# Performance work log

Measured on AMD Instinct MI355X. Metric: run time of the kernel, lower is better.

The kernel has to match this reference:

```python
import jax, jax.numpy as jnp
import numpy as np

WINDOW = 8  # outlier_fraction = 0.125 -> 1 fp column kept per 8-wide window

# XnorBinaryLinear's STEBinary: sign in fwd, identity (straight-through) in bwd
@jax.custom_vjp
def ste_sign(x):
    return jnp.sign(x)

def _ste_fwd(x):
    return jnp.sign(x), None

def _ste_bwd(_, g):
    return (g,)

ste_sign.defvjp(_ste_fwd, _ste_bwd)


def quant_weight(w):
    # XnorBinaryLinear.quant_weight: per-row mean-center, sign, rescale by
    # detached per-row mean absolute value
    mu = jnp.mean(w, axis=-1, keepdims=True)
    wc = w - mu
    scale = jax.lax.stop_gradient(jnp.mean(jnp.abs(wc), axis=-1, keepdims=True))
    return ste_sign(wc) * scale


def binarize_except_outliers(w):
    # Binarize weight, then restore the max-|w| element of each flat 8-wide
    # window to full precision (calibration = argmax of |w| per window,
    # identical to outlier_calibration with L1 metric on first forward).
    wq = quant_weight(w)
    wv = w.reshape(-1, WINDOW)             # [n_windows, 8]
    idx = jnp.argmax(jnp.abs(wv), axis=1)  # [n_windows] outlier column per window
    mask = jnp.arange(WINDOW)[None, :] == idx[:, None]  # one-hot bool mask
    out = jnp.where(mask, wv, wq.reshape(-1, WINDOW))
    return out.reshape(w.shape)


def setup_inputs() -> dict:
    key = jax.random.key(0)
    k1, k2, k3 = jax.random.split(key, 3)
    x = jax.random.normal(k1, (4, 2048, 4096), dtype=jnp.float32)
    weight = jax.random.normal(k2, (4096, 4096), dtype=jnp.float32) * 0.02
    bias = jax.random.normal(k3, (4096,), dtype=jnp.float32) * 0.02
    return {"x": x, "weight": weight, "bias": bias}


def reference(x, weight, bias):
    w = binarize_except_outliers(weight)     # [OC, IC]
    return jnp.einsum('bsi,oi->bso', x, w) + bias
```

## Files before the change

### kernel.cpp

```cpp
#include <hip/hip_runtime.h>
#include <stdint.h>

#define M_DIM 8192
#define N_DIM 4096
#define K_DIM 4096

#define BM 256
#define BN 128
#define BK 32
#define NT (K_DIM / BK)

typedef float v4f __attribute__((ext_vector_type(4)));
typedef __bf16 v8bf __attribute__((ext_vector_type(8)));

typedef __attribute__((address_space(3))) uint32_t lds_u32_t;
typedef const __attribute__((address_space(1))) uint32_t glb_u32_t;

__device__ inline uint16_t f2bf(float f) {
    union { float f; uint32_t u; } v; v.f = f;
    uint32_t r = v.u + 0x7fffu + ((v.u >> 16) & 1u);
    return (uint16_t)(r >> 16);
}

__global__ __launch_bounds__(256) void cvt_x(const float* __restrict__ x,
                                             uint16_t* __restrict__ xb,
                                             long long n4) {
    long long stride = (long long)gridDim.x * 256;
    for (long long i = (long long)blockIdx.x * 256 + threadIdx.x; i < n4; i += stride) {
        float4 a = ((const float4*)x)[i];
        union { uint16_t h[4]; uint2 u; } o;
        o.h[0] = f2bf(a.x); o.h[1] = f2bf(a.y); o.h[2] = f2bf(a.z); o.h[3] = f2bf(a.w);
        ((uint2*)xb)[i] = o.u;
    }
}

__global__ __launch_bounds__(256) void make_weff(const float* __restrict__ w,
                                                 uint16_t* __restrict__ weff) {
    __shared__ double red[4];
    int row  = blockIdx.x;
    int tid  = threadIdx.x;
    int lane = tid & 63;
    int wid  = tid >> 6;

    const float* wr = w + (size_t)row * K_DIM;
    const float4* w4 = (const float4*)wr + tid * 4;
    float4 r0 = w4[0], r1 = w4[1], r2 = w4[2], r3 = w4[3];
    float v[16] = { r0.x, r0.y, r0.z, r0.w, r1.x, r1.y, r1.z, r1.w,
                    r2.x, r2.y, r2.z, r2.w, r3.x, r3.y, r3.z, r3.w };

    double s = 0.0;
#pragma unroll
    for (int j = 0; j < 16; j++) s += (double)v[j];
#pragma unroll
    for (int off = 32; off > 0; off >>= 1) s += __shfl_down(s, off);
    if (lane == 0) red[wid] = s;
    __syncthreads();
    double mu = (red[0] + red[1] + red[2] + red[3]) * (1.0 / 4096.0);
    __syncthreads();

    double sa = 0.0;
#pragma unroll
    for (int j = 0; j < 16; j++) sa += fabs((double)v[j] - mu);
#pragma unroll
    for (int off = 32; off > 0; off >>= 1) sa += __shfl_down(sa, off);
    if (lane == 0) red[wid] = sa;
    __syncthreads();
    double scale = (red[0] + red[1] + red[2] + red[3]) * (1.0 / 4096.0);

    float scf = (float)scale;
    union { uint16_t h[16]; uint4 u[2]; } o;
#pragma unroll
    for (int w2 = 0; w2 < 2; w2++) {
        int base = w2 * 8;
        int amax = 0;
        float mx = fabsf(v[base]);
#pragma unroll
        for (int j = 1; j < 8; j++) {
            float aj = fabsf(v[base + j]);
            if (aj > mx) { mx = aj; amax = j; }
        }
#pragma unroll
        for (int j = 0; j < 8; j++) {
            double wc = (double)v[base + j] - mu;
            float q = (wc > 0.0) ? scf : ((wc < 0.0) ? -scf : 0.0f);
            o.h[base + j] = f2bf((j == amax) ? v[base + j] : q);
        }
    }
    uint4* dst = (uint4*)(weff + (size_t)row * K_DIM + (size_t)tid * 16);
    dst[0] = o.u[0];
    dst[1] = o.u[1];
}


__device__ inline void async_cp16(const uint16_t* g, uint16_t* lds_uniform) {
    __builtin_amdgcn_global_load_lds((glb_u32_t*)g, (lds_u32_t*)lds_uniform, 16, 0, 0);
}

__device__ __forceinline__ void load4(v8bf (&d)[4], const uint16_t* base) {
#pragma unroll
    for (int i = 0; i < 4; ++i) d[i] = *(const v8bf*)(base + i * 512);
}

#define BAR  __builtin_amdgcn_s_barrier()
#define PRIO1 __builtin_amdgcn_s_setprio(1)
#define PRIO0 __builtin_amdgcn_s_setprio(0)
#define VMWAIT(N) asm volatile("s_waitcnt vmcnt(" #N ")" ::: "memory")

#define STG_A(BUFV, KOFF) do { \
    async_cp16(a_s0 + (KOFF), ldsA + (BUFV) * 8192 + wid * 1024);       \
    async_cp16(a_s1 + (KOFF), ldsA + (BUFV) * 8192 + wid * 1024 + 512); \
} while (0)
#define STG_B(BUFV, KOFF) do { \
    async_cp16(b_s0 + (KOFF), ldsB + (BUFV) * 4096 + wid * 512);        \
} while (0)

#define TILE1(BUFV, KNEXT)                                                     \
  {                                                                            \
    v8bf aF[4], bF[4];                                                         \
    load4(aF, rdA + (BUFV) * 8192);                                            \
    load4(bF, rdB + (BUFV) * 4096);                                            \
    STG_A(1 - (BUFV), KNEXT);                                                  \
    STG_B(1 - (BUFV), KNEXT);                                                  \
    PRIO1;                                                                     \
    _Pragma("unroll")                                                          \
    for (int fm = 0; fm < 4; ++fm)                                             \
      _Pragma("unroll")                                                        \
      for (int fn = 0; fn < 4; ++fn)                                           \
        acc[fm][fn] = __builtin_amdgcn_mfma_f32_16x16x32_bf16(aF[fm], bF[fn],  \
                                                              acc[fm][fn], 0, 0, 0); \
    PRIO0;                                                                     \
    VMWAIT(0);                                                                 \
    BAR;                                                                       \
  }

__global__ __launch_bounds__(512, 4) void gemm_bt(const uint16_t* __restrict__ A,
                                                  const uint16_t* __restrict__ B,
                                                  const float* __restrict__ bias,
                                                  float* __restrict__ C) {
    __shared__ __attribute__((aligned(128))) uint16_t ldsA[2 * 8192];
    __shared__ __attribute__((aligned(128))) uint16_t ldsB[2 * 4096];

    int tid  = threadIdx.x;
    int lane = tid & 63;
    int wid  = tid >> 6;
    int wm   = wid >> 1;
    int wn   = wid & 1;

    int bid = blockIdx.x;
    int swz = (bid & 7) * 128 + (bid >> 3);
    long long bm = (long long)(swz >> 5) * BM;
    long long bn = (long long)(swz & 31) * BN;

    int srow = lane >> 2;
    int scs  = (lane & 3) ^ ((srow >> 1) & 3);
    const uint16_t* a_s0 = A + (size_t)(bm + wid * 32 +  0 + srow) * K_DIM + scs * 8;
    const uint16_t* a_s1 = A + (size_t)(bm + wid * 32 + 16 + srow) * K_DIM + scs * 8;
    const uint16_t* b_s0 = B + (size_t)(bn + wid * 16 +       srow) * K_DIM + scs * 8;

    int rl   = lane & 15;
    int aoff = rl * 32 + (((lane >> 4) ^ ((rl >> 1) & 3)) * 8);
    const uint16_t* rdA = ldsA + wm * 2048 + aoff;
    const uint16_t* rdB = ldsB + wn * 2048 + aoff;

    v4f acc[4][4];
#pragma unroll
    for (int i = 0; i < 4; ++i)
#pragma unroll
        for (int j = 0; j < 4; ++j) acc[i][j] = (v4f)(0.0f);

    STG_A(0, 0);
    STG_B(0, 0);
    VMWAIT(0);
    BAR;

#pragma clang loop unroll(disable)
    for (int it = 0; it < NT / 2; ++it) {
        int t2 = it * 2;
        int k1 = (t2 + 1) * BK;
        int k2 = (t2 + 2 < NT) ? (t2 + 2) * BK : t2 * BK;
        TILE1(0, k1);
        TILE1(1, k2);
    }

    int cl = lane & 15;
    int ch = lane >> 4;
#pragma unroll
    for (int fn = 0; fn < 4; ++fn) {
        int n = (int)bn + wn * 64 + fn * 16 + cl;
        float bj = bias[n];
#pragma unroll
        for (int fm = 0; fm < 4; ++fm) {
            size_t rbase = (size_t)(bm + wm * 64 + fm * 16 + ch * 4) * N_DIM + n;
#pragma unroll
            for (int g = 0; g < 4; ++g)
                C[rbase + (size_t)g * N_DIM] = acc[fm][fn][g] + bj;
        }
    }
}

extern "C" void kernel_launch(void* const* d_in, const int* in_sizes, int n_in,
                              void* d_out, int out_size, void* d_ws, size_t ws_size,
                              hipStream_t stream) {
    const float* x    = (const float*)d_in[0];
    const float* w    = (const float*)d_in[1];
    const float* bias = (const float*)d_in[2];
    float* out = (float*)d_out;

    uint16_t* xb   = (uint16_t*)d_ws;
    uint16_t* weff = (uint16_t*)((char*)d_ws + (size_t)M_DIM * K_DIM * 2);

    long long n4 = (long long)M_DIM * K_DIM / 4;
    cvt_x<<<dim3(4096), dim3(256), 0, stream>>>(x, xb, n4);
    make_weff<<<dim3(N_DIM), dim3(256), 0, stream>>>(w, weff);
    gemm_bt<<<dim3((M_DIM / BM) * (N_DIM / BN)), dim3(512), 0, stream>>>(xb, weff, bias, out);
}
```

Measured before the change: 549.6 us.

## Replace direct global-to-LDS copies with register-staged prefetch two tiles ahead

```diff
diff --git a/kernel.cpp b/kernel.cpp
--- a/kernel.cpp
+++ b/kernel.cpp
@@ -12,9 +12,6 @@
 
 typedef float v4f __attribute__((ext_vector_type(4)));
 typedef __bf16 v8bf __attribute__((ext_vector_type(8)));
-
-typedef __attribute__((address_space(3))) uint32_t lds_u32_t;
-typedef const __attribute__((address_space(1))) uint32_t glb_u32_t;
 
 __device__ inline uint16_t f2bf(float f) {
     union { float f; uint32_t u; } v; v.f = f;
@@ -92,46 +89,15 @@
 }
 
 
-__device__ inline void async_cp16(const uint16_t* g, uint16_t* lds_uniform) {
-    __builtin_amdgcn_global_load_lds((glb_u32_t*)g, (lds_u32_t*)lds_uniform, 16, 0, 0);
-}
-
-__device__ __forceinline__ void load4(v8bf (&d)[4], const uint16_t* base) {
-#pragma unroll
-    for (int i = 0; i < 4; ++i) d[i] = *(const v8bf*)(base + i * 512);
-}
-
 #define BAR  __builtin_amdgcn_s_barrier()
 #define PRIO1 __builtin_amdgcn_s_setprio(1)
 #define PRIO0 __builtin_amdgcn_s_setprio(0)
-#define VMWAIT(N) asm volatile("s_waitcnt vmcnt(" #N ")" ::: "memory")
-
-#define STG_A(BUFV, KOFF) do { \
-    async_cp16(a_s0 + (KOFF), ldsA + (BUFV) * 8192 + wid * 1024);       \
-    async_cp16(a_s1 + (KOFF), ldsA + (BUFV) * 8192 + wid * 1024 + 512); \
-} while (0)
-#define STG_B(BUFV, KOFF) do { \
-    async_cp16(b_s0 + (KOFF), ldsB + (BUFV) * 4096 + wid * 512);        \
-} while (0)
-
-#define TILE1(BUFV, KNEXT)                                                     \
-  {                                                                            \
-    v8bf aF[4], bF[4];                                                         \
-    load4(aF, rdA + (BUFV) * 8192);                                            \
-    load4(bF, rdB + (BUFV) * 4096);                                            \
-    STG_A(1 - (BUFV), KNEXT);                                                  \
-    STG_B(1 - (BUFV), KNEXT);                                                  \
-    PRIO1;                                                                     \
-    _Pragma("unroll")                                                          \
-    for (int fm = 0; fm < 4; ++fm)                                             \
-      _Pragma("unroll")                                                        \
-      for (int fn = 0; fn < 4; ++fn)                                           \
-        acc[fm][fn] = __builtin_amdgcn_mfma_f32_16x16x32_bf16(aF[fm], bF[fn],  \
-                                                              acc[fm][fn], 0, 0, 0); \
-    PRIO0;                                                                     \
-    VMWAIT(0);                                                                 \
-    BAR;                                                                       \
-  }
+#define LGKM0 asm volatile("s_waitcnt lgkmcnt(0)" ::: "memory")
+
+__device__ __forceinline__ void load4(v8bf (&d)[4], const uint16_t* base) {
+#pragma unroll
+    for (int i = 0; i < 4; ++i) d[i] = *(const v8bf*)(base + i * 512);
+}
 
 __global__ __launch_bounds__(512, 4) void gemm_bt(const uint16_t* __restrict__ A,
                                                   const uint16_t* __restrict__ B,
@@ -157,6 +123,10 @@
     const uint16_t* a_s1 = A + (size_t)(bm + wid * 32 + 16 + srow) * K_DIM + scs * 8;
     const uint16_t* b_s0 = B + (size_t)(bn + wid * 16 +       srow) * K_DIM + scs * 8;
 
+    uint16_t* wA0 = ldsA + (wid * 32 +  0 + srow) * 32 + (lane & 3) * 8;
+    uint16_t* wA1 = ldsA + (wid * 32 + 16 + srow) * 32 + (lane & 3) * 8;
+    uint16_t* wB  = ldsB + (wid * 16 +       srow) * 32 + (lane & 3) * 8;
+
     int rl   = lane & 15;
     int aoff = rl * 32 + (((lane >> 4) ^ ((rl >> 1) & 3)) * 8);
     const uint16_t* rdA = ldsA + wm * 2048 + aoff;
@@ -168,18 +138,53 @@
 #pragma unroll
         for (int j = 0; j < 4; ++j) acc[i][j] = (v4f)(0.0f);
 
-    STG_A(0, 0);
-    STG_B(0, 0);
-    VMWAIT(0);
+    uint4 g0, g1, g2;
+
+    g0 = *(const uint4*)a_s0; g1 = *(const uint4*)a_s1; g2 = *(const uint4*)b_s0;
+    *(uint4*)wA0 = g0; *(uint4*)wA1 = g1; *(uint4*)wB = g2;
+    g0 = *(const uint4*)(a_s0 + BK); g1 = *(const uint4*)(a_s1 + BK); g2 = *(const uint4*)(b_s0 + BK);
+    LGKM0;
     BAR;
 
-#pragma clang loop unroll(disable)
-    for (int it = 0; it < NT / 2; ++it) {
-        int t2 = it * 2;
-        int k1 = (t2 + 1) * BK;
-        int k2 = (t2 + 2 < NT) ? (t2 + 2) * BK : t2 * BK;
-        TILE1(0, k1);
-        TILE1(1, k2);
+#pragma clang loop unroll_count(2)
+    for (int t = 0; t < NT - 1; ++t) {
+        int bo  = (t & 1);
+        int boN = bo ^ 1;
+        *(uint4*)(wA0 + boN * 8192) = g0;
+        *(uint4*)(wA1 + boN * 8192) = g1;
+        *(uint4*)(wB  + boN * 4096) = g2;
+        int kk = ((t + 2 < NT) ? (t + 2) : (NT - 1)) * BK;
+        g0 = *(const uint4*)(a_s0 + kk);
+        g1 = *(const uint4*)(a_s1 + kk);
+        g2 = *(const uint4*)(b_s0 + kk);
+        {
+            v8bf aF[4], bF[4];
+            load4(aF, rdA + bo * 8192);
+            load4(bF, rdB + bo * 4096);
+            PRIO1;
+#pragma unroll
+            for (int fm = 0; fm < 4; ++fm)
+#pragma unroll
+                for (int fn = 0; fn < 4; ++fn)
+                    acc[fm][fn] = __builtin_amdgcn_mfma_f32_16x16x32_bf16(aF[fm], bF[fn],
+                                                                          acc[fm][fn], 0, 0, 0);
+            PRIO0;
+        }
+        LGKM0;
+        BAR;
+    }
+    {
+        v8bf aF[4], bF[4];
+        load4(aF, rdA + 8192);
+        load4(bF, rdB + 4096);
+        PRIO1;
+#pragma unroll
+        for (int fm = 0; fm < 4; ++fm)
+#pragma unroll
+            for (int fn = 0; fn < 4; ++fn)
+                acc[fm][fn] = __builtin_amdgcn_mfma_f32_16x16x32_bf16(aF[fm], bF[fn],
+                                                                      acc[fm][fn], 0, 0, 0);
+        PRIO0;
     }
 
     int cl = lane & 15;
```

Result: no change. 553.9 us (+0.8%).
